# Kernel tuning notes

Measured on AMD Instinct MI355X. Metric: run time of the kernel, lower is better.

## Reference

```python
import jax, jax.numpy as jnp
import numpy as np

# Gating config (matches init_kwargs)
N_GROUPS = 4        # n_expert_groups
TOPK_GROUPS = 2     # n_limited_groups
TOPK = 4            # n_activated_experts
ROUTE_SCALE = 1.0


def setup_inputs() -> dict:
    key = jax.random.key(0)
    ks = jax.random.split(key, 8)
    T, D, E, I = 2048, 1024, 16, 512
    s = 0.02  # init scale for sane numerics
    return {
        "x": jax.random.normal(ks[0], (T, D), jnp.float32),
        "gate_w": jax.random.normal(ks[1], (E, D), jnp.float32) * s,
        "w1": jax.random.normal(ks[2], (E, I, D), jnp.float32) * s,
        "w2": jax.random.normal(ks[3], (E, D, I), jnp.float32) * s,
        "w3": jax.random.normal(ks[4], (E, I, D), jnp.float32) * s,
        "ws1": jax.random.normal(ks[5], (I, D), jnp.float32) * s,
        "ws2": jax.random.normal(ks[6], (D, I), jnp.float32) * s,
        "ws3": jax.random.normal(ks[7], (I, D), jnp.float32) * s,
    }


def _gate(x, gate_w):
    # GateDeepSeekV3.forward: softmax scores, group-limited routing, top-k experts.
    T = x.shape[0]
    scores = jax.nn.softmax((x @ gate_w.T).astype(jnp.float32), axis=-1)  # [T, E]
    original_scores = scores
    E = scores.shape[-1]
    # group-limited routing: keep top `TOPK_GROUPS` groups by max score (bias is None)
    s = scores.reshape(T, N_GROUPS, E // N_GROUPS)
    group_scores = s.max(axis=-1)                                  # [T, G]
    _, gidx = jax.lax.top_k(group_scores, TOPK_GROUPS)             # [T, Gk]
    mask = jnp.zeros((T, N_GROUPS), scores.dtype).at[jnp.arange(T)[:, None], gidx].set(1.0)
    s = (s * mask[:, :, None]).reshape(T, E)
    _, indices = jax.lax.top_k(s, TOPK)                            # [T, topk]
    weights = jnp.take_along_axis(original_scores, indices, axis=1) * ROUTE_SCALE
    return weights.astype(x.dtype), indices


def reference(x, gate_w, w1, w2, w3, ws1, ws2, ws3):
    T, D = x.shape
    E = w1.shape[0]
    weights, indices = _gate(x, gate_w)
    # dense [T, E] combine weights (topk indices are unique per token)
    gate_dense = jnp.zeros((T, E), x.dtype).at[jnp.arange(T)[:, None], indices].add(weights)
    # routed experts: y_t = sum_e g[t,e] * W2_e (silu(W1_e x) * (W3_e x))
    h = jax.nn.silu(jnp.einsum('td,eid->tei', x, w1)) * jnp.einsum('td,eid->tei', x, w3)
    y = jnp.einsum('tei,te,edi->td', h, gate_dense, w2)
    # shared expert MLP over all tokens
    z = (jax.nn.silu(x @ ws1.T) * (x @ ws3.T)) @ ws2.T
    return y + z
```

## Files before the change

kernel.cpp:

```cpp
#include <hip/hip_runtime.h>
#include <hip/hip_bf16.h>
#include <math.h>

typedef float v4f __attribute__((ext_vector_type(4)));
typedef short v8s __attribute__((ext_vector_type(8)));

#define T_TOK   2048
#define DDIM    1024
#define NE      16
#define IDIM    512
#define S_ROUTED 8192
#define S_ALL   10240
#define MAXTILE 104

#define OFF_TOPKI    0u
#define OFF_TOPKW    32768u
#define OFF_PART     65536u
#define OFF_CBASE    69632u
#define OFF_SEGOFF   73728u
#define OFF_NTILES   74240u
#define OFF_TROW     74752u
#define OFF_TEND     75776u
#define OFF_TEXP     76800u
#define OFF_SLOTWT   81920u
#define OFF_S2T      114688u
#define OFF_SLOTOF   155648u
#define OFF_XBF      (1u<<20)
#define OFF_H        (8u<<20)
#define OFF_YP       (24u<<20)

__device__ __forceinline__ unsigned short f2bf(float f) {
    unsigned int u = __float_as_uint(f);
    unsigned int r = (u + 0x7fffu + ((u >> 16) & 1u)) >> 16;
    return (unsigned short)r;
}
__device__ __forceinline__ float bf2f(unsigned short s) {
    return __uint_as_float((unsigned)s << 16);
}
__device__ __forceinline__ unsigned cvt2(float lo, float hi) {
    unsigned r;
    asm("v_cvt_pk_bf16_f32 %0, %1, %2" : "=v"(r) : "v"(lo), "v"(hi));
    return r;
}

#define GLL16(gp, lp) __builtin_amdgcn_global_load_lds( \
    (__attribute__((address_space(1))) void*)(gp), \
    (__attribute__((address_space(3))) void*)(lp), 16, 0, 0)

__global__ __launch_bounds__(256) void gate_kernel(
    const float* __restrict__ x, const float* __restrict__ gw,
    int* __restrict__ topki, float* __restrict__ topkw,
    unsigned short* __restrict__ xbf)
{
    int t = blockIdx.x;
    int tid = threadIdx.x, lane = tid & 63, wave = tid >> 6;
    const float4* xr = (const float4*)(x + (size_t)t * DDIM);
    float4 xv[4];
#pragma unroll
    for (int j = 0; j < 4; j++) xv[j] = xr[lane + 64 * j];

    __shared__ float sc[NE];
#pragma unroll
    for (int ee = 0; ee < 4; ee++) {
        int e = wave * 4 + ee;
        const float4* wr = (const float4*)(gw + (size_t)e * DDIM);
        float acc = 0.f;
#pragma unroll
        for (int j = 0; j < 4; j++) {
            float4 w = wr[lane + 64 * j];
            acc += xv[j].x * w.x + xv[j].y * w.y + xv[j].z * w.z + xv[j].w * w.w;
        }
#pragma unroll
        for (int off = 32; off; off >>= 1) acc += __shfl_down(acc, off, 64);
        if (lane == 0) sc[e] = acc;
    }
    if (wave == 0) {
#pragma unroll
        for (int j = 0; j < 4; j++) {
            int base = 4 * (lane + 64 * j);
            uint2 p;
            p.x = (unsigned)f2bf(xv[j].x) | ((unsigned)f2bf(xv[j].y) << 16);
            p.y = (unsigned)f2bf(xv[j].z) | ((unsigned)f2bf(xv[j].w) << 16);
            *(uint2*)(xbf + (size_t)t * DDIM + base) = p;
        }
    }
    __syncthreads();
    if (tid == 0) {
        float mx = sc[0];
#pragma unroll
        for (int e = 1; e < NE; e++) mx = fmaxf(mx, sc[e]);
        float sco[NE]; float sum = 0.f;
#pragma unroll
        for (int e = 0; e < NE; e++) { sco[e] = __expf(sc[e] - mx); sum += sco[e]; }
        float inv = 1.f / sum;
#pragma unroll
        for (int e = 0; e < NE; e++) sco[e] *= inv;
        float gs[4];
#pragma unroll
        for (int g = 0; g < 4; g++) {
            float m = sco[4 * g];
            m = fmaxf(m, sco[4 * g + 1]); m = fmaxf(m, sco[4 * g + 2]); m = fmaxf(m, sco[4 * g + 3]);
            gs[g] = m;
        }
        int g0 = 0;
        for (int g = 1; g < 4; g++) if (gs[g] > gs[g0]) g0 = g;
        int g1 = -1;
        for (int g = 0; g < 4; g++) { if (g == g0) continue; if (g1 < 0 || gs[g] > gs[g1]) g1 = g; }
        float ms[NE];
#pragma unroll
        for (int e = 0; e < NE; e++) {
            int g = e >> 2;
            ms[e] = (g == g0 || g == g1) ? sco[e] : 0.0f;
        }
        bool used[NE] = {false};
        for (int k = 0; k < 4; k++) {
            int best = -1;
            for (int e = 0; e < NE; e++) {
                if (used[e]) continue;
                if (best < 0 || ms[e] > ms[best]) best = e;
            }
            used[best] = true;
            topki[t * 4 + k] = best;
            topkw[t * 4 + k] = sco[best];
        }
    }
}

__global__ __launch_bounds__(256) void hist_kernel(
    const int* __restrict__ topki, int* __restrict__ part)
{
    __shared__ int cnt[16];
    int tid = threadIdx.x, b = blockIdx.x;
    if (tid < 16) cnt[tid] = 0;
    __syncthreads();
    int e = topki[b * 256 + tid];
    int lane = tid & 63;
#pragma unroll
    for (int e0 = 0; e0 < 16; e0++) {
        unsigned long long mask = __ballot(e == e0);
        if (lane == 0) atomicAdd(&cnt[e0], __popcll(mask));
    }
    __syncthreads();
    if (tid < 16) part[b * 16 + tid] = cnt[tid];
}

__global__ __launch_bounds__(256) void scan_kernel(
    const int* __restrict__ part, int* __restrict__ cbase, int* __restrict__ segoff,
    int* __restrict__ trow, int* __restrict__ tend, int* __restrict__ texp,
    int* __restrict__ ntp)
{
    int tid = threadIdx.x;
    __shared__ int tot[16];
    __shared__ int so[17];
    if (tid < 16) {
        int s = 0;
        for (int b = 0; b < 32; b++) s += part[b * 16 + tid];
        tot[tid] = s;
    }
    __syncthreads();
    if (tid == 0) {
        int off = 0;
        for (int e = 0; e < 16; e++) { so[e] = off; segoff[e] = off; off += tot[e]; }
        so[16] = off; segoff[16] = off; segoff[17] = off + T_TOK;
        int nt = 0;
        for (int e = 0; e < 17; e++) {
            int n = (e < 16) ? tot[e] : T_TOK;
            int base = (e < 16) ? so[e] : S_ROUTED;
            for (int m = 0; m < n; m += 128) {
                trow[nt] = base + m; tend[nt] = base + n; texp[nt] = e; nt++;
            }
        }
        *ntp = nt;
    }
    __syncthreads();
    if (tid < 16) {
        int run = so[tid];
        for (int b = 0; b < 32; b++) { cbase[b * 16 + tid] = run; run += part[b * 16 + tid]; }
    }
}

__global__ __launch_bounds__(256) void assign_kernel(
    const int* __restrict__ topki, const float* __restrict__ topkw,
    const int* __restrict__ cbase, int* __restrict__ s2t,
    float* __restrict__ slotwt, int* __restrict__ slotof)
{
    int b = blockIdx.x, tid = threadIdx.x;
    int i = b * 256 + tid;
    int e = topki[i];
    int lane = tid & 63, wave = tid >> 6;
    __shared__ int wcnt[4][16];
    int lrank = 0;
#pragma unroll
    for (int e0 = 0; e0 < 16; e0++) {
        unsigned long long mask = __ballot(e == e0);
        if (e == e0) lrank = __popcll(mask & ((1ull << lane) - 1ull));
        if (lane == 0) wcnt[wave][e0] = __popcll(mask);
    }
    __syncthreads();
    int pre = 0;
    for (int w = 0; w < wave; w++) pre += wcnt[w][e];
    int slot = cbase[b * 16 + e] + pre + lrank;
    int t = i >> 2;
    s2t[slot] = t;
    slotwt[slot] = topkw[i];
    slotof[i] = slot;
    if ((i & 3) == 0) s2t[S_ROUTED + t] = t;
}

__global__ __launch_bounds__(256, 3) void gemm1_kernel(
    const float* __restrict__ w1, const float* __restrict__ w3,
    const float* __restrict__ s1, const float* __restrict__ s3,
    const unsigned short* __restrict__ xbf,
    unsigned short* __restrict__ h, const float* __restrict__ slotwt,
    const int* __restrict__ s2t,
    const int* __restrict__ trow, const int* __restrict__ tend,
    const int* __restrict__ texp, const int* __restrict__ ntp)
{
    int bid = blockIdx.x;
    int tile = bid >> 3, ct = bid & 7;
    if (tile >= *ntp) return;
    int row0 = trow[tile], rend = tend[tile], e = texp[tile];
    int n0 = ct * 64;
    const float* B1 = (e < 16) ? (w1 + (size_t)e * 524288) : s1;
    const float* B3 = (e < 16) ? (w3 + (size_t)e * 524288) : s3;

    __shared__ __align__(16) short As[2][128 * 64];
    __shared__ __align__(16) short Bs[128 * 64];

    int tid = threadIdx.x;
    int lane = tid & 63, wave = tid >> 6;
    int wm = wave & 1, wn = wave >> 1;
    int mq = lane >> 4, nl = lane & 15;
    int rr = lane >> 3, cbl = (lane & 7) ^ rr;

    const unsigned short* asrc[4];
#pragma unroll
    for (int j = 0; j < 4; j++)
        asrc[j] = xbf + (size_t)s2t[row0 + wave * 32 + j * 8 + rr] * DDIM + cbl * 8;

    const float* bsrc[4];
    int boff[4];
#pragma unroll
    for (int j = 0; j < 4; j++) {
        int u = tid + 256 * j;
        int brow = u >> 3, bblk = u & 7;
        boff[j] = brow * 64 + ((bblk ^ (brow & 7)) * 8);
        int half = brow >> 6;
        const float* base = half ? B3 : B1;
        bsrc[j] = base + (size_t)(n0 + (brow & 63)) * DDIM + bblk * 8;
    }

    v4f acc[4][4];
#pragma unroll
    for (int i = 0; i < 4; i++)
#pragma unroll
        for (int j = 0; j < 4; j++) acc[i][j] = (v4f)0.f;

    float4 br0[4], br1[4];
#pragma unroll
    for (int j = 0; j < 4; j++) {
        br0[j] = *(const float4*)(bsrc[j]);
        br1[j] = *(const float4*)(bsrc[j] + 4);
    }
#pragma unroll
    for (int j = 0; j < 4; j++)
        GLL16(asrc[j], (short*)As[0] + wave * 2048 + j * 512);

    for (int ki = 0; ki < 16; ki++) {
        __syncthreads();
#pragma unroll
        for (int j = 0; j < 4; j++) {
            uint4 p;
            p.x = cvt2(br0[j].x, br0[j].y);
            p.y = cvt2(br0[j].z, br0[j].w);
            p.z = cvt2(br1[j].x, br1[j].y);
            p.w = cvt2(br1[j].z, br1[j].w);
            *(uint4*)(Bs + boff[j]) = p;
        }
        __syncthreads();
        if (ki < 15) {
            int kc = (ki + 1) * 64;
#pragma unroll
            for (int j = 0; j < 4; j++)
                GLL16(asrc[j] + kc, (short*)As[(ki + 1) & 1] + wave * 2048 + j * 512);
#pragma unroll
            for (int j = 0; j < 4; j++) {
                br0[j] = *(const float4*)(bsrc[j] + kc);
                br1[j] = *(const float4*)(bsrc[j] + kc + 4);
            }
        }
        const short* Acur = (const short*)As[ki & 1];
#pragma unroll
        for (int ks = 0; ks < 2; ks++) {
            int kb = ks * 4 + mq;
            v8s a[4], b[4];
#pragma unroll
            for (int mi = 0; mi < 4; mi++) {
                int R = wm * 64 + mi * 16 + nl;
                a[mi] = *(const v8s*)(Acur + R * 64 + ((kb ^ (nl & 7)) * 8));
            }
#pragma unroll
            for (int ni = 0; ni < 4; ni++) {
                int S = (ni >> 1) * 64 + wn * 32 + (ni & 1) * 16 + nl;
                b[ni] = *(const v8s*)(Bs + S * 64 + ((kb ^ (nl & 7)) * 8));
            }
#pragma unroll
            for (int mi = 0; mi < 4; mi++)
#pragma unroll
                for (int ni = 0; ni < 4; ni++)
                    acc[mi][ni] = __builtin_amdgcn_mfma_f32_16x16x32_bf16(a[mi], b[ni], acc[mi][ni], 0, 0, 0);
        }
    }
#pragma unroll
    for (int mi = 0; mi < 4; mi++) {
#pragma unroll
        for (int r = 0; r < 4; r++) {
            int srow = row0 + wm * 64 + mi * 16 + mq * 4 + r;
            if (srow < rend) {
                float g = (srow < S_ROUTED) ? slotwt[srow] : 1.0f;
#pragma unroll
                for (int ni = 0; ni < 2; ni++) {
                    float p1 = acc[mi][ni][r], p3 = acc[mi][ni + 2][r];
                    float sig = 1.f / (1.f + __expf(-p1));
                    h[(size_t)srow * IDIM + n0 + wn * 32 + ni * 16 + nl] = f2bf(p1 * sig * p3 * g);
                }
            }
        }
    }
}

__global__ __launch_bounds__(256, 3) void gemm2_kernel(
    const float* __restrict__ w2, const float* __restrict__ s2w,
    const unsigned short* __restrict__ h, unsigned short* __restrict__ yp,
    const int* __restrict__ trow, const int* __restrict__ tend,
    const int* __restrict__ texp, const int* __restrict__ ntp)
{
    int bid = blockIdx.x;
    int tile = bid >> 3, ct = bid & 7;
    if (tile >= *ntp) return;
    int row0 = trow[tile], rend = tend[tile], e = texp[tile];
    int n0 = ct * 128;
    const float* B = ((e < 16) ? (w2 + (size_t)e * 524288) : s2w) + (size_t)n0 * IDIM;

    __shared__ __align__(16) short As[2][128 * 64];
    __shared__ __align__(16) short Bs[128 * 64];

    int tid = threadIdx.x;
    int lane = tid & 63, wave = tid >> 6;
    int wm = wave & 1, wn = wave >> 1;
    int mq = lane >> 4, nl = lane & 15;
    int rr = lane >> 3, cbl = (lane & 7) ^ rr;

    const unsigned short* asrc[4];
#pragma unroll
    for (int j = 0; j < 4; j++)
        asrc[j] = h + (size_t)(row0 + wave * 32 + j * 8 + rr) * IDIM + cbl * 8;

    const float* bsrc[4];
    int boff[4];
#pragma unroll
    for (int j = 0; j < 4; j++) {
        int u = tid + 256 * j;
        int brow = u >> 3, bblk = u & 7;
        boff[j] = brow * 64 + ((bblk ^ (brow & 7)) * 8);
        bsrc[j] = B + (size_t)brow * IDIM + bblk * 8;
    }

    v4f acc[4][4];
#pragma unroll
    for (int i = 0; i < 4; i++)
#pragma unroll
        for (int j = 0; j < 4; j++) acc[i][j] = (v4f)0.f;

    float4 br0[4], br1[4];
#pragma unroll
    for (int j = 0; j < 4; j++) {
        br0[j] = *(const float4*)(bsrc[j]);
        br1[j] = *(const float4*)(bsrc[j] + 4);
    }
#pragma unroll
    for (int j = 0; j < 4; j++)
        GLL16(asrc[j], (short*)As[0] + wave * 2048 + j * 512);

    for (int ki = 0; ki < 8; ki++) {
        __syncthreads();
#pragma unroll
        for (int j = 0; j < 4; j++) {
            uint4 p;
            p.x = cvt2(br0[j].x, br0[j].y);
            p.y = cvt2(br0[j].z, br0[j].w);
            p.z = cvt2(br1[j].x, br1[j].y);
            p.w = cvt2(br1[j].z, br1[j].w);
            *(uint4*)(Bs + boff[j]) = p;
        }
        __syncthreads();
        if (ki < 7) {
            int kc = (ki + 1) * 64;
#pragma unroll
            for (int j = 0; j < 4; j++)
                GLL16(asrc[j] + kc, (short*)As[(ki + 1) & 1] + wave * 2048 + j * 512);
#pragma unroll
            for (int j = 0; j < 4; j++) {
                br0[j] = *(const float4*)(bsrc[j] + kc);
                br1[j] = *(const float4*)(bsrc[j] + kc + 4);
            }
        }
        const short* Acur = (const short*)As[ki & 1];
#pragma unroll
        for (int ks = 0; ks < 2; ks++) {
            int kb = ks * 4 + mq;
            v8s a[4], b[4];
#pragma unroll
            for (int mi = 0; mi < 4; mi++) {
                int R = wm * 64 + mi * 16 + nl;
                a[mi] = *(const v8s*)(Acur + R * 64 + ((kb ^ (nl & 7)) * 8));
            }
#pragma unroll
            for (int ni = 0; ni < 4; ni++) {
                int S = wn * 64 + ni * 16 + nl;
                b[ni] = *(const v8s*)(Bs + S * 64 + ((kb ^ (nl & 7)) * 8));
            }
#pragma unroll
            for (int mi = 0; mi < 4; mi++)
#pragma unroll
                for (int ni = 0; ni < 4; ni++)
                    acc[mi][ni] = __builtin_amdgcn_mfma_f32_16x16x32_bf16(a[mi], b[ni], acc[mi][ni], 0, 0, 0);
        }
    }
#pragma unroll
    for (int mi = 0; mi < 4; mi++) {
#pragma unroll
        for (int r = 0; r < 4; r++) {
            int srow = row0 + wm * 64 + mi * 16 + mq * 4 + r;
            if (srow < rend) {
                unsigned short* yrow = yp + ((size_t)srow << 10) + n0 + wn * 64 + nl;
#pragma unroll
                for (int ni = 0; ni < 4; ni++)
                    yrow[ni * 16] = f2bf(acc[mi][ni][r]);
            }
        }
    }
}

__global__ __launch_bounds__(256) void combine_kernel(
    const unsigned short* __restrict__ yp, const int* __restrict__ slotof,
    float* __restrict__ out)
{
    int t = blockIdx.x;
    int c = threadIdx.x * 4;
    int s0 = slotof[t * 4 + 0], s1 = slotof[t * 4 + 1];
    int s2 = slotof[t * 4 + 2], s3 = slotof[t * 4 + 3];
    ushort4 v  = *(const ushort4*)(yp + (((size_t)(S_ROUTED + t)) << 10) + c);
    ushort4 a0 = *(const ushort4*)(yp + (((size_t)s0) << 10) + c);
    ushort4 a1 = *(const ushort4*)(yp + (((size_t)s1) << 10) + c);
    ushort4 a2 = *(const ushort4*)(yp + (((size_t)s2) << 10) + c);
    ushort4 a3 = *(const ushort4*)(yp + (((size_t)s3) << 10) + c);
    float4 o;
    o.x = bf2f(v.x) + bf2f(a0.x) + bf2f(a1.x) + bf2f(a2.x) + bf2f(a3.x);
    o.y = bf2f(v.y) + bf2f(a0.y) + bf2f(a1.y) + bf2f(a2.y) + bf2f(a3.y);
    o.z = bf2f(v.z) + bf2f(a0.z) + bf2f(a1.z) + bf2f(a2.z) + bf2f(a3.z);
    o.w = bf2f(v.w) + bf2f(a0.w) + bf2f(a1.w) + bf2f(a2.w) + bf2f(a3.w);
    *(float4*)(out + (((size_t)t) << 10) + c) = o;
}

extern "C" void kernel_launch(void* const* d_in, const int* in_sizes, int n_in,
                              void* d_out, int out_size, void* d_ws, size_t ws_size,
                              hipStream_t stream) {
    const float* x    = (const float*)d_in[0];
    const float* gw   = (const float*)d_in[1];
    const float* w1   = (const float*)d_in[2];
    const float* w2   = (const float*)d_in[3];
    const float* w3   = (const float*)d_in[4];
    const float* wsh1 = (const float*)d_in[5];
    const float* wsh2 = (const float*)d_in[6];
    const float* wsh3 = (const float*)d_in[7];
    float* out = (float*)d_out;

    char* ws = (char*)d_ws;
    int*   topki  = (int*)(ws + OFF_TOPKI);
    float* topkw  = (float*)(ws + OFF_TOPKW);
    int*   part   = (int*)(ws + OFF_PART);
    int*   cbase  = (int*)(ws + OFF_CBASE);
    int*   segoff = (int*)(ws + OFF_SEGOFF);
    int*   ntp    = (int*)(ws + OFF_NTILES);
    int*   trow   = (int*)(ws + OFF_TROW);
    int*   tend   = (int*)(ws + OFF_TEND);
    int*   texp   = (int*)(ws + OFF_TEXP);
    float* slotwt = (float*)(ws + OFF_SLOTWT);
    int*   s2t    = (int*)(ws + OFF_S2T);
    int*   slotof = (int*)(ws + OFF_SLOTOF);
    unsigned short* xbf = (unsigned short*)(ws + OFF_XBF);
    unsigned short* h   = (unsigned short*)(ws + OFF_H);
    unsigned short* yp  = (unsigned short*)(ws + OFF_YP);

    gate_kernel<<<T_TOK, 256, 0, stream>>>(x, gw, topki, topkw, xbf);
    hist_kernel<<<32, 256, 0, stream>>>(topki, part);
    scan_kernel<<<1, 256, 0, stream>>>(part, cbase, segoff, trow, tend, texp, ntp);
    assign_kernel<<<32, 256, 0, stream>>>(topki, topkw, cbase, s2t, slotwt, slotof);
    gemm1_kernel<<<MAXTILE * 8, 256, 0, stream>>>(w1, w3, wsh1, wsh3, xbf, h, slotwt, s2t,
                                                  trow, tend, texp, ntp);
    gemm2_kernel<<<MAXTILE * 8, 256, 0, stream>>>(w2, wsh2, h, yp, trow, tend, texp, ntp);
    combine_kernel<<<T_TOK, 256, 0, stream>>>(yp, slotof, out);
}
```

Baseline: 227.3 us.

## Shrink M tile to 64 rows and drop A double-buffering in expert GEMMs

Routed-expert tiles go from 128 to 64 token rows, which roughly doubles the number of blocks and cuts padding waste on partially filled expert segments. Each wave now covers all 64 rows and a 16- or 32-column slice. The A operand is single-buffered and loaded at the top of each k-step, and launch bounds rise to 4 blocks per CU. In exchange, every fp32 weight tile is now read and converted twice as often, and the A loads are no longer prefetched ahead of the MFMA work.

```diff
diff --git a/kernel.cpp b/kernel.cpp
--- a/kernel.cpp
+++ b/kernel.cpp
@@ -11,7 +11,7 @@
 #define IDIM    512
 #define S_ROUTED 8192
 #define S_ALL   10240
-#define MAXTILE 104
+#define MAXTILE 200
 
 #define OFF_TOPKI    0u
 #define OFF_TOPKW    32768u
@@ -166,7 +166,7 @@
         for (int e = 0; e < 17; e++) {
             int n = (e < 16) ? tot[e] : T_TOK;
             int base = (e < 16) ? so[e] : S_ROUTED;
-            for (int m = 0; m < n; m += 128) {
+            for (int m = 0; m < n; m += 64) {
                 trow[nt] = base + m; tend[nt] = base + n; texp[nt] = e; nt++;
             }
         }
@@ -207,7 +207,7 @@
     if ((i & 3) == 0) s2t[S_ROUTED + t] = t;
 }
 
-__global__ __launch_bounds__(256, 3) void gemm1_kernel(
+__global__ __launch_bounds__(256, 4) void gemm1_kernel(
     const float* __restrict__ w1, const float* __restrict__ w3,
     const float* __restrict__ s1, const float* __restrict__ s3,
     const unsigned short* __restrict__ xbf,
@@ -224,19 +224,18 @@
     const float* B1 = (e < 16) ? (w1 + (size_t)e * 524288) : s1;
     const float* B3 = (e < 16) ? (w3 + (size_t)e * 524288) : s3;
 
-    __shared__ __align__(16) short As[2][128 * 64];
+    __shared__ __align__(16) short As[64 * 64];
     __shared__ __align__(16) short Bs[128 * 64];
 
     int tid = threadIdx.x;
-    int lane = tid & 63, wave = tid >> 6;
-    int wm = wave & 1, wn = wave >> 1;
+    int lane = tid & 63, wv = tid >> 6;
     int mq = lane >> 4, nl = lane & 15;
     int rr = lane >> 3, cbl = (lane & 7) ^ rr;
 
-    const unsigned short* asrc[4];
-#pragma unroll
-    for (int j = 0; j < 4; j++)
-        asrc[j] = xbf + (size_t)s2t[row0 + wave * 32 + j * 8 + rr] * DDIM + cbl * 8;
+    const unsigned short* asrc[2];
+#pragma unroll
+    for (int j = 0; j < 2; j++)
+        asrc[j] = xbf + (size_t)s2t[row0 + wv * 16 + j * 8 + rr] * DDIM + cbl * 8;
 
     const float* bsrc[4];
     int boff[4];
@@ -250,11 +249,11 @@
         bsrc[j] = base + (size_t)(n0 + (brow & 63)) * DDIM + bblk * 8;
     }
 
-    v4f acc[4][4];
+    v4f acc[4][2];
 #pragma unroll
     for (int i = 0; i < 4; i++)
 #pragma unroll
-        for (int j = 0; j < 4; j++) acc[i][j] = (v4f)0.f;
+        for (int j = 0; j < 2; j++) acc[i][j] = (v4f)0.f;
 
     float4 br0[4], br1[4];
 #pragma unroll
@@ -262,12 +261,13 @@
         br0[j] = *(const float4*)(bsrc[j]);
         br1[j] = *(const float4*)(bsrc[j] + 4);
     }
-#pragma unroll
-    for (int j = 0; j < 4; j++)
-        GLL16(asrc[j], (short*)As[0] + wave * 2048 + j * 512);
 
     for (int ki = 0; ki < 16; ki++) {
+        int kc = ki * 64;
         __syncthreads();
+#pragma unroll
+        for (int j = 0; j < 2; j++)
+            GLL16(asrc[j] + kc, As + wv * 1024 + j * 512);
 #pragma unroll
         for (int j = 0; j < 4; j++) {
             uint4 p;
@@ -279,57 +279,46 @@
         }
         __syncthreads();
         if (ki < 15) {
-            int kc = (ki + 1) * 64;
-#pragma unroll
-            for (int j = 0; j < 4; j++)
-                GLL16(asrc[j] + kc, (short*)As[(ki + 1) & 1] + wave * 2048 + j * 512);
 #pragma unroll
             for (int j = 0; j < 4; j++) {
-                br0[j] = *(const float4*)(bsrc[j] + kc);
-                br1[j] = *(const float4*)(bsrc[j] + kc + 4);
-            }
-        }
-        const short* Acur = (const short*)As[ki & 1];
+                br0[j] = *(const float4*)(bsrc[j] + kc + 64);
+                br1[j] = *(const float4*)(bsrc[j] + kc + 68);
+            }
+        }
 #pragma unroll
         for (int ks = 0; ks < 2; ks++) {
             int kb = ks * 4 + mq;
-            v8s a[4], b[4];
+            v8s a[4], b1, b3;
 #pragma unroll
             for (int mi = 0; mi < 4; mi++) {
-                int R = wm * 64 + mi * 16 + nl;
-                a[mi] = *(const v8s*)(Acur + R * 64 + ((kb ^ (nl & 7)) * 8));
-            }
-#pragma unroll
-            for (int ni = 0; ni < 4; ni++) {
-                int S = (ni >> 1) * 64 + wn * 32 + (ni & 1) * 16 + nl;
-                b[ni] = *(const v8s*)(Bs + S * 64 + ((kb ^ (nl & 7)) * 8));
-            }
-#pragma unroll
-            for (int mi = 0; mi < 4; mi++)
-#pragma unroll
-                for (int ni = 0; ni < 4; ni++)
-                    acc[mi][ni] = __builtin_amdgcn_mfma_f32_16x16x32_bf16(a[mi], b[ni], acc[mi][ni], 0, 0, 0);
+                int R = mi * 16 + nl;
+                a[mi] = *(const v8s*)(As + R * 64 + ((kb ^ (nl & 7)) * 8));
+            }
+            b1 = *(const v8s*)(Bs + (wv * 16 + nl) * 64 + ((kb ^ (nl & 7)) * 8));
+            b3 = *(const v8s*)(Bs + (64 + wv * 16 + nl) * 64 + ((kb ^ (nl & 7)) * 8));
+#pragma unroll
+            for (int mi = 0; mi < 4; mi++) {
+                acc[mi][0] = __builtin_amdgcn_mfma_f32_16x16x32_bf16(a[mi], b1, acc[mi][0], 0, 0, 0);
+                acc[mi][1] = __builtin_amdgcn_mfma_f32_16x16x32_bf16(a[mi], b3, acc[mi][1], 0, 0, 0);
+            }
         }
     }
 #pragma unroll
     for (int mi = 0; mi < 4; mi++) {
 #pragma unroll
         for (int r = 0; r < 4; r++) {
-            int srow = row0 + wm * 64 + mi * 16 + mq * 4 + r;
+            int srow = row0 + mi * 16 + mq * 4 + r;
             if (srow < rend) {
                 float g = (srow < S_ROUTED) ? slotwt[srow] : 1.0f;
-#pragma unroll
-                for (int ni = 0; ni < 2; ni++) {
-                    float p1 = acc[mi][ni][r], p3 = acc[mi][ni + 2][r];
-                    float sig = 1.f / (1.f + __expf(-p1));
-                    h[(size_t)srow * IDIM + n0 + wn * 32 + ni * 16 + nl] = f2bf(p1 * sig * p3 * g);
-                }
-            }
-        }
-    }
-}
-
-__global__ __launch_bounds__(256, 3) void gemm2_kernel(
+                float p1 = acc[mi][0][r], p3 = acc[mi][1][r];
+                float sig = 1.f / (1.f + __expf(-p1));
+                h[(size_t)srow * IDIM + n0 + wv * 16 + nl] = f2bf(p1 * sig * p3 * g);
+            }
+        }
+    }
+}
+
+__global__ __launch_bounds__(256, 4) void gemm2_kernel(
     const float* __restrict__ w2, const float* __restrict__ s2w,
     const unsigned short* __restrict__ h, unsigned short* __restrict__ yp,
     const int* __restrict__ trow, const int* __restrict__ tend,
@@ -342,19 +331,18 @@
     int n0 = ct * 128;
     const float* B = ((e < 16) ? (w2 + (size_t)e * 524288) : s2w) + (size_t)n0 * IDIM;
 
-    __shared__ __align__(16) short As[2][128 * 64];
+    __shared__ __align__(16) short As[64 * 64];
     __shared__ __align__(16) short Bs[128 * 64];
 
     int tid = threadIdx.x;
-    int lane = tid & 63, wave = tid >> 6;
-    int wm = wave & 1, wn = wave >> 1;
+    int lane = tid & 63, wv = tid >> 6;
     int mq = lane >> 4, nl = lane & 15;
     int rr = lane >> 3, cbl = (lane & 7) ^ rr;
 
-    const unsigned short* asrc[4];
-#pragma unroll
-    for (int j = 0; j < 4; j++)
-        asrc[j] = h + (size_t)(row0 + wave * 32 + j * 8 + rr) * IDIM + cbl * 8;
+    const unsigned short* asrc[2];
+#pragma unroll
+    for (int j = 0; j < 2; j++)
+        asrc[j] = h + (size_t)(row0 + wv * 16 + j * 8 + rr) * IDIM + cbl * 8;
 
     const float* bsrc[4];
     int boff[4];
@@ -366,11 +354,11 @@
         bsrc[j] = B + (size_t)brow * IDIM + bblk * 8;
     }
 
-    v4f acc[4][4];
+    v4f acc[4][2];
 #pragma unroll
     for (int i = 0; i < 4; i++)
 #pragma unroll
-        for (int j = 0; j < 4; j++) acc[i][j] = (v4f)0.f;
+        for (int j = 0; j < 2; j++) acc[i][j] = (v4f)0.f;
 
     float4 br0[4], br1[4];
 #pragma unroll
@@ -378,12 +366,13 @@
         br0[j] = *(const float4*)(bsrc[j]);
         br1[j] = *(const float4*)(bsrc[j] + 4);
     }
-#pragma unroll
-    for (int j = 0; j < 4; j++)
-        GLL16(asrc[j], (short*)As[0] + wave * 2048 + j * 512);
 
     for (int ki = 0; ki < 8; ki++) {
+        int kc = ki * 64;
         __syncthreads();
+#pragma unroll
+        for (int j = 0; j < 2; j++)
+            GLL16(asrc[j] + kc, As + wv * 1024 + j * 512);
 #pragma unroll
         for (int j = 0; j < 4; j++) {
             uint4 p;
@@ -395,35 +384,30 @@
         }
         __syncthreads();
         if (ki < 7) {
-            int kc = (ki + 1) * 64;
-#pragma unroll
-            for (int j = 0; j < 4; j++)
-                GLL16(asrc[j] + kc, (short*)As[(ki + 1) & 1] + wave * 2048 + j * 512);
 #pragma unroll
             for (int j = 0; j < 4; j++) {
-                br0[j] = *(const float4*)(bsrc[j] + kc);
-                br1[j] = *(const float4*)(bsrc[j] + kc + 4);
-            }
-        }
-        const short* Acur = (const short*)As[ki & 1];
+                br0[j] = *(const float4*)(bsrc[j] + kc + 64);
+                br1[j] = *(const float4*)(bsrc[j] + kc + 68);
+            }
+        }
 #pragma unroll
         for (int ks = 0; ks < 2; ks++) {
             int kb = ks * 4 + mq;
-            v8s a[4], b[4];
+            v8s a[4], b[2];
 #pragma unroll
             for (int mi = 0; mi < 4; mi++) {
-                int R = wm * 64 + mi * 16 + nl;
-                a[mi] = *(const v8s*)(Acur + R * 64 + ((kb ^ (nl & 7)) * 8));
-            }
-#pragma unroll
-            for (int ni = 0; ni < 4; ni++) {
-                int S = wn * 64 + ni * 16 + nl;
+                int R = mi * 16 + nl;
+                a[mi] = *(const v8s*)(As + R * 64 + ((kb ^ (nl & 7)) * 8));
+            }
+#pragma unroll
+            for (int ni = 0; ni < 2; ni++) {
+                int S = wv * 32 + ni * 16 + nl;
                 b[ni] = *(const v8s*)(Bs + S * 64 + ((kb ^ (nl & 7)) * 8));
             }
 #pragma unroll
             for (int mi = 0; mi < 4; mi++)
 #pragma unroll
-                for (int ni = 0; ni < 4; ni++)
+                for (int ni = 0; ni < 2; ni++)
                     acc[mi][ni] = __builtin_amdgcn_mfma_f32_16x16x32_bf16(a[mi], b[ni], acc[mi][ni], 0, 0, 0);
         }
     }
@@ -431,11 +415,11 @@
     for (int mi = 0; mi < 4; mi++) {
 #pragma unroll
         for (int r = 0; r < 4; r++) {
-            int srow = row0 + wm * 64 + mi * 16 + mq * 4 + r;
+            int srow = row0 + mi * 16 + mq * 4 + r;
             if (srow < rend) {
-                unsigned short* yrow = yp + ((size_t)srow << 10) + n0 + wn * 64 + nl;
-#pragma unroll
-                for (int ni = 0; ni < 4; ni++)
+                unsigned short* yrow = yp + ((size_t)srow << 10) + n0 + wv * 32 + nl;
+#pragma unroll
+                for (int ni = 0; ni < 2; ni++)
                     yrow[ni * 16] = f2bf(acc[mi][ni][r]);
             }
         }
```

Measured after the change: 254.2 us. +11.8%, slower.

## Load A fragments directly from global and double-buffer B tile in LDS

Applied to the files above, without the earlier changes.

Both GEMM kernels stop staging the activation (A) tile in LDS through global_load_lds. Each wave now reads its MFMA A fragments straight from global memory, so A rows are fetched by both wn waves. The single B buffer becomes double-buffered: the next K-slice is converted to bf16 and written into the other buffer after the MFMAs, which removes one __syncthreads per iteration. This trades more global/L2 traffic and exposed A-load latency inside the MFMA loop for fewer barriers and less LDS use, which may allow higher occupancy.

```diff
diff --git a/kernel.cpp b/kernel.cpp
--- a/kernel.cpp
+++ b/kernel.cpp
@@ -43,10 +43,6 @@
     return r;
 }
 
-#define GLL16(gp, lp) __builtin_amdgcn_global_load_lds( \
-    (__attribute__((address_space(1))) void*)(gp), \
-    (__attribute__((address_space(3))) void*)(lp), 16, 0, 0)
-
 __global__ __launch_bounds__(256) void gate_kernel(
     const float* __restrict__ x, const float* __restrict__ gw,
     int* __restrict__ topki, float* __restrict__ topkw,
@@ -224,19 +220,17 @@
     const float* B1 = (e < 16) ? (w1 + (size_t)e * 524288) : s1;
     const float* B3 = (e < 16) ? (w3 + (size_t)e * 524288) : s3;
 
-    __shared__ __align__(16) short As[2][128 * 64];
-    __shared__ __align__(16) short Bs[128 * 64];
+    __shared__ __align__(16) short Bs[2][128 * 64];
 
     int tid = threadIdx.x;
     int lane = tid & 63, wave = tid >> 6;
     int wm = wave & 1, wn = wave >> 1;
     int mq = lane >> 4, nl = lane & 15;
-    int rr = lane >> 3, cbl = (lane & 7) ^ rr;
-
-    const unsigned short* asrc[4];
-#pragma unroll
-    for (int j = 0; j < 4; j++)
-        asrc[j] = xbf + (size_t)s2t[row0 + wave * 32 + j * 8 + rr] * DDIM + cbl * 8;
+
+    const unsigned short* abase[4];
+#pragma unroll
+    for (int mi = 0; mi < 4; mi++)
+        abase[mi] = xbf + (size_t)s2t[row0 + wm * 64 + mi * 16 + nl] * DDIM + mq * 8;
 
     const float* bsrc[4];
     int boff[4];
@@ -263,46 +257,38 @@
         br1[j] = *(const float4*)(bsrc[j] + 4);
     }
 #pragma unroll
-    for (int j = 0; j < 4; j++)
-        GLL16(asrc[j], (short*)As[0] + wave * 2048 + j * 512);
-
+    for (int j = 0; j < 4; j++) {
+        uint4 p;
+        p.x = cvt2(br0[j].x, br0[j].y);
+        p.y = cvt2(br0[j].z, br0[j].w);
+        p.z = cvt2(br1[j].x, br1[j].y);
+        p.w = cvt2(br1[j].z, br1[j].w);
+        *(uint4*)((short*)Bs[0] + boff[j]) = p;
+    }
+
+    int cur = 0;
     for (int ki = 0; ki < 16; ki++) {
-        __syncthreads();
-#pragma unroll
-        for (int j = 0; j < 4; j++) {
-            uint4 p;
-            p.x = cvt2(br0[j].x, br0[j].y);
-            p.y = cvt2(br0[j].z, br0[j].w);
-            p.z = cvt2(br1[j].x, br1[j].y);
-            p.w = cvt2(br1[j].z, br1[j].w);
-            *(uint4*)(Bs + boff[j]) = p;
-        }
+        int kc = ki * 64;
         __syncthreads();
         if (ki < 15) {
-            int kc = (ki + 1) * 64;
-#pragma unroll
-            for (int j = 0; j < 4; j++)
-                GLL16(asrc[j] + kc, (short*)As[(ki + 1) & 1] + wave * 2048 + j * 512);
 #pragma unroll
             for (int j = 0; j < 4; j++) {
-                br0[j] = *(const float4*)(bsrc[j] + kc);
-                br1[j] = *(const float4*)(bsrc[j] + kc + 4);
-            }
-        }
-        const short* Acur = (const short*)As[ki & 1];
+                br0[j] = *(const float4*)(bsrc[j] + kc + 64);
+                br1[j] = *(const float4*)(bsrc[j] + kc + 68);
+            }
+        }
+        const short* Bc = (const short*)Bs[cur];
 #pragma unroll
         for (int ks = 0; ks < 2; ks++) {
             int kb = ks * 4 + mq;
             v8s a[4], b[4];
 #pragma unroll
-            for (int mi = 0; mi < 4; mi++) {
-                int R = wm * 64 + mi * 16 + nl;
-                a[mi] = *(const v8s*)(Acur + R * 64 + ((kb ^ (nl & 7)) * 8));
-            }
+            for (int mi = 0; mi < 4; mi++)
+                a[mi] = *(const v8s*)(abase[mi] + kc + ks * 32);
 #pragma unroll
             for (int ni = 0; ni < 4; ni++) {
                 int S = (ni >> 1) * 64 + wn * 32 + (ni & 1) * 16 + nl;
-                b[ni] = *(const v8s*)(Bs + S * 64 + ((kb ^ (nl & 7)) * 8));
+                b[ni] = *(const v8s*)(Bc + S * 64 + ((kb ^ (nl & 7)) * 8));
             }
 #pragma unroll
             for (int mi = 0; mi < 4; mi++)
@@ -310,6 +296,18 @@
                 for (int ni = 0; ni < 4; ni++)
                     acc[mi][ni] = __builtin_amdgcn_mfma_f32_16x16x32_bf16(a[mi], b[ni], acc[mi][ni], 0, 0, 0);
         }
+        if (ki < 15) {
+#pragma unroll
+            for (int j = 0; j < 4; j++) {
+                uint4 p;
+                p.x = cvt2(br0[j].x, br0[j].y);
+                p.y = cvt2(br0[j].z, br0[j].w);
+                p.z = cvt2(br1[j].x, br1[j].y);
+                p.w = cvt2(br1[j].z, br1[j].w);
+                *(uint4*)((short*)Bs[cur ^ 1] + boff[j]) = p;
+            }
+        }
+        cur ^= 1;
     }
 #pragma unroll
     for (int mi = 0; mi < 4; mi++) {
@@ -342,19 +340,17 @@
     int n0 = ct * 128;
     const float* B = ((e < 16) ? (w2 + (size_t)e * 524288) : s2w) + (size_t)n0 * IDIM;
 
-    __shared__ __align__(16) short As[2][128 * 64];
-    __shared__ __align__(16) short Bs[128 * 64];
+    __shared__ __align__(16) short Bs[2][128 * 64];
 
     int tid = threadIdx.x;
     int lane = tid & 63, wave = tid >> 6;
     int wm = wave & 1, wn = wave >> 1;
     int mq = lane >> 4, nl = lane & 15;
-    int rr = lane >> 3, cbl = (lane & 7) ^ rr;
-
-    const unsigned short* asrc[4];
-#pragma unroll
-    for (int j = 0; j < 4; j++)
-        asrc[j] = h + (size_t)(row0 + wave * 32 + j * 8 + rr) * IDIM + cbl * 8;
+
+    const unsigned short* abase[4];
+#pragma unroll
+    for (int mi = 0; mi < 4; mi++)
+        abase[mi] = h + (size_t)(row0 + wm * 64 + mi * 16 + nl) * IDIM + mq * 8;
 
     const float* bsrc[4];
     int boff[4];
@@ -379,46 +375,38 @@
         br1[j] = *(const float4*)(bsrc[j] + 4);
     }
 #pragma unroll
-    for (int j = 0; j < 4; j++)
-        GLL16(asrc[j], (short*)As[0] + wave * 2048 + j * 512);
-
+    for (int j = 0; j < 4; j++) {
+        uint4 p;
+        p.x = cvt2(br0[j].x, br0[j].y);
+        p.y = cvt2(br0[j].z, br0[j].w);
+        p.z = cvt2(br1[j].x, br1[j].y);
+        p.w = cvt2(br1[j].z, br1[j].w);
+        *(uint4*)((short*)Bs[0] + boff[j]) = p;
+    }
+
+    int cur = 0;
     for (int ki = 0; ki < 8; ki++) {
-        __syncthreads();
-#pragma unroll
-        for (int j = 0; j < 4; j++) {
-            uint4 p;
-            p.x = cvt2(br0[j].x, br0[j].y);
-            p.y = cvt2(br0[j].z, br0[j].w);
-            p.z = cvt2(br1[j].x, br1[j].y);
-            p.w = cvt2(br1[j].z, br1[j].w);
-            *(uint4*)(Bs + boff[j]) = p;
-        }
+        int kc = ki * 64;
         __syncthreads();
         if (ki < 7) {
-            int kc = (ki + 1) * 64;
-#pragma unroll
-            for (int j = 0; j < 4; j++)
-                GLL16(asrc[j] + kc, (short*)As[(ki + 1) & 1] + wave * 2048 + j * 512);
 #pragma unroll
             for (int j = 0; j < 4; j++) {
-                br0[j] = *(const float4*)(bsrc[j] + kc);
-                br1[j] = *(const float4*)(bsrc[j] + kc + 4);
-            }
-        }
-        const short* Acur = (const short*)As[ki & 1];
+                br0[j] = *(const float4*)(bsrc[j] + kc + 64);
+                br1[j] = *(const float4*)(bsrc[j] + kc + 68);
+            }
+        }
+        const short* Bc = (const short*)Bs[cur];
 #pragma unroll
         for (int ks = 0; ks < 2; ks++) {
             int kb = ks * 4 + mq;
             v8s a[4], b[4];
 #pragma unroll
-            for (int mi = 0; mi < 4; mi++) {
-                int R = wm * 64 + mi * 16 + nl;
-                a[mi] = *(const v8s*)(Acur + R * 64 + ((kb ^ (nl & 7)) * 8));
-            }
+            for (int mi = 0; mi < 4; mi++)
+                a[mi] = *(const v8s*)(abase[mi] + kc + ks * 32);
 #pragma unroll
             for (int ni = 0; ni < 4; ni++) {
                 int S = wn * 64 + ni * 16 + nl;
-                b[ni] = *(const v8s*)(Bs + S * 64 + ((kb ^ (nl & 7)) * 8));
+                b[ni] = *(const v8s*)(Bc + S * 64 + ((kb ^ (nl & 7)) * 8));
             }
 #pragma unroll
             for (int mi = 0; mi < 4; mi++)
@@ -426,6 +414,18 @@
                 for (int ni = 0; ni < 4; ni++)
                     acc[mi][ni] = __builtin_amdgcn_mfma_f32_16x16x32_bf16(a[mi], b[ni], acc[mi][ni], 0, 0, 0);
         }
+        if (ki < 7) {
+#pragma unroll
+            for (int j = 0; j < 4; j++) {
+                uint4 p;
+                p.x = cvt2(br0[j].x, br0[j].y);
+                p.y = cvt2(br0[j].z, br0[j].w);
+                p.z = cvt2(br1[j].x, br1[j].y);
+                p.w = cvt2(br1[j].z, br1[j].w);
+                *(uint4*)((short*)Bs[cur ^ 1] + boff[j]) = p;
+            }
+        }
+        cur ^= 1;
     }
 #pragma unroll
     for (int mi = 0; mi < 4; mi++) {
```

Result: slower. 256.2 us (+12.7%).
